# Optimization experiments

Measured on AMD Instinct MI355X. Metric: run time of the kernel, lower is better.

The kernel has to match this reference:

```python
import jax, jax.numpy as jnp
import numpy as np

WS = 7          # window_size
HEADS = 3
HD = 32         # head_dim
HIDDEN = 96
DISP = WS // 2  # 3
NEG_INF = float('-inf')


def _relative_indices():
    idx = np.array([[i, j] for i in range(WS) for j in range(WS)])
    rel = idx[None, :, :] - idx[:, None, :] + WS - 1  # [49,49,2], values in [0, 2*WS-2]
    return rel.astype(np.int32)


def _upper_lower_mask():
    m = np.zeros((WS * WS, WS * WS), dtype=np.float32)
    m[-DISP * WS:, :-DISP * WS] = NEG_INF
    m[:-DISP * WS, -DISP * WS:] = NEG_INF
    return m


def setup_inputs() -> dict:
    key = jax.random.key(0)
    ks = jax.random.split(key, 6)
    B, H, W = 32, 56, 56
    inner = HEADS * HD
    return {
        'x': jax.random.normal(ks[0], (B, H, W, HIDDEN), jnp.float32),
        'w_qkv': jax.random.normal(ks[1], (HIDDEN, inner * 3), jnp.float32) * 0.05,
        'b_qkv': jax.random.normal(ks[2], (inner * 3,), jnp.float32) * 0.05,
        'pos_embedding': jax.random.normal(ks[3], (2 * WS - 1, 2 * WS - 1), jnp.float32),
        'w_out': jax.random.normal(ks[4], (inner, HIDDEN), jnp.float32) * 0.05,
        'b_out': jax.random.normal(ks[5], (HIDDEN,), jnp.float32) * 0.05,
    }


def reference(x, w_qkv, b_qkv, pos_embedding, w_out, b_out):
    B, H, W, _ = x.shape
    nw_h, nw_w = H // WS, W // WS
    nw = nw_h * nw_w
    scale = HIDDEN ** (-0.5)  # original scales by hidden_dim**-0.5

    rel = jnp.asarray(_relative_indices())
    ul_mask = jnp.asarray(_upper_lower_mask())

    # cyclic shift
    xs = jnp.roll(x, (-DISP, -DISP), axis=(1, 2))
    qkv = xs @ w_qkv + b_qkv
    q, k, v = jnp.split(qkv, 3, axis=-1)

    def to_windows(e):
        # [B,H,W,heads*hd] -> [B,heads,nw,WS*WS,hd]
        e = e.reshape(B, nw_h, WS, nw_w, WS, HEADS, HD)
        e = e.transpose(0, 5, 1, 3, 2, 4, 6)
        return e.reshape(B, HEADS, nw, WS * WS, HD)

    q, k, v = to_windows(q), to_windows(k), to_windows(v)

    att = jnp.einsum('bhwid,bhwjd->bhwij', q, k) * scale
    att = att + pos_embedding[rel[:, :, 0], rel[:, :, 1]]
    # shifted: original only adds upper_lower_mask (right_left line is a no-op bug)
    att = att.at[:, :, -nw_w:].add(ul_mask)
    att = jax.nn.softmax(att, axis=-1)

    out = jnp.einsum('bhwij,bhwjd->bhwid', att, v)
    out = out.reshape(B, HEADS, nw_h, nw_w, WS, WS, HD)
    out = out.transpose(0, 2, 4, 3, 5, 1, 6).reshape(B, H, W, HEADS * HD)
    out = out @ w_out + b_out
    out = jnp.roll(out, (DISP, DISP), axis=(1, 2))
    return out
```

## Files before the change

kernel.cpp:

```cpp
#include <hip/hip_runtime.h>
#include <hip/hip_bf16.h>
#include <cmath>

using bf16 = __hip_bfloat16;
typedef __attribute__((ext_vector_type(8))) short short8;
typedef __attribute__((ext_vector_type(4))) float floatx4;

#define B_      32
#define HH      56
#define WW      56
#define HIDDEN  96
#define HEADS   3
#define HD      32
#define WS_     7
#define DISP    3
#define NWH     8
#define NWW     8
#define NW      64
#define WS2     49
#define NFRAG_QKV (3*6*3*64)
#define NFRAG_OUT (6*3*64)
#define NPEL      (2*64*64)

#if __has_builtin(__builtin_amdgcn_exp2f)
#define EXP2(x) __builtin_amdgcn_exp2f(x)
#else
#define EXP2(x) exp2f(x)
#endif

__device__ inline unsigned short bf16_bits(float f) {
  unsigned u = __float_as_uint(f);
  unsigned r = u + 0x7fffu + ((u >> 16) & 1u);
  return (unsigned short)(r >> 16);
}

__device__ inline unsigned cvtpk(float lo, float hi) {
  unsigned r;
  asm("v_cvt_pk_bf16_f32 %0, %1, %2" : "=v"(r) : "v"(lo), "v"(hi));
  return r;
}

__device__ inline unsigned short* swz(const unsigned short* plane, int row, int boff) {
  return (unsigned short*)((char*)plane + (row << 6) + (boff ^ ((row & 3) << 4)));
}

__global__ __launch_bounds__(256) void prep_kernel(
    const float* __restrict__ w_qkv, const float* __restrict__ w_out,
    const float* __restrict__ pos_emb,
    bf16* __restrict__ wfq, bf16* __restrict__ wfo, float* __restrict__ pelT) {
  int f = blockIdx.x * 256 + threadIdx.x;
  if (f < NFRAG_QKV) {
    int lane = f & 63, t = f >> 6;
    int kb = t % 3, t2 = t / 3, c6 = t2 % 6, ci = t2 / 6;
    int col = ci * 96 + c6 * 16 + (lane & 15);
    int k0 = kb * 32 + (lane >> 4) * 8;
    bf16 vals[8];
#pragma unroll
    for (int j = 0; j < 8; j++) vals[j] = __float2bfloat16(w_qkv[(k0 + j) * 288 + col]);
    *(short8*)&wfq[(size_t)f * 8] = *(const short8*)vals;
  } else if (f < NFRAG_QKV + NFRAG_OUT) {
    int fo = f - NFRAG_QKV;
    int lane = fo & 63, t = fo >> 6;
    int kb = t % 3, c6 = t / 3;
    int col = c6 * 16 + (lane & 15);
    int k0 = kb * 32 + (lane >> 4) * 8;
    bf16 vals[8];
#pragma unroll
    for (int j = 0; j < 8; j++) vals[j] = __float2bfloat16(w_out[(k0 + j) * 96 + col]);
    *(short8*)&wfo[(size_t)fo * 8] = *(const short8*)vals;
  } else {
    int p = f - (NFRAG_QKV + NFRAG_OUT);
    if (p < NPEL) {
      int mk = p >> 12, i = (p >> 6) & 63, j = p & 63;
      int iy = i / WS_, ix = i % WS_, jy = j / WS_, jx = j % WS_;
      int idx = (jy - iy + 6) * 13 + (jx - ix + 6);
      idx = idx < 0 ? 0 : (idx > 168 ? 168 : idx);
      bool live = (i < WS2) && (j < WS2) && !(mk && ((i >= 28) != (j >= 28)));
      pelT[p] = live ? pos_emb[idx] * 1.4426950408889634f : -1e30f;
    }
  }
}

__global__ __launch_bounds__(256, 4) void fused_swin_kernel(
    const float* __restrict__ x,
    const bf16* __restrict__ wfq, const bf16* __restrict__ wfo,
    const float* __restrict__ b_qkv, const float* __restrict__ b_out,
    const float* __restrict__ pelT, float* __restrict__ out) {

  __shared__ unsigned short slabA[3][64][32];
  __shared__ unsigned short slabB[3][64][32];
  __shared__ unsigned short vT[3][32][72];
  __shared__ unsigned tokoff[64];

  const int blk = blockIdx.x;
  const int nw = blk & 63, b = blk >> 6;
  const int wy = nw >> 3, wx = nw & 7;
  const int tid = threadIdx.x;
  const int lane = tid & 63, wv = tid >> 6;
  const int n_ = lane & 15, quad = lane >> 4;

  const short8* wfQ = (const short8*)wfq;
  short8 wcur0 = wfQ[(size_t)((wv * 3 + 0) * 64 + lane)];
  short8 wcur1 = wfQ[(size_t)((wv * 3 + 1) * 64 + lane)];
  short8 wcur2 = wfQ[(size_t)((wv * 3 + 2) * 64 + lane)];

  {
    const int rowp = tid >> 2, s0 = tid & 3;
    const bool haveRow = rowp < WS2;
    const float* xrow = x;
    if (haveRow) {
      const int py = rowp / WS_, px = rowp % WS_;
      int h = wy * WS_ + py + DISP; if (h >= HH) h -= HH;
      int w = wx * WS_ + px + DISP; if (w >= WW) w -= WW;
      const unsigned toff = (unsigned)(((b * HH + h) * WW + w) * HIDDEN);
      xrow = x + toff;
      if (s0 == 0) tokoff[rowp] = toff;
    }
#pragma unroll
    for (int p = 0; p < 6; p++) {
      const int seg = s0 + 4 * p;
      const int kb = seg >> 3;
      uint2 pk = (uint2){0u, 0u};
      if (haveRow) {
        const float4 xv = *(const float4*)&xrow[seg * 4];
        pk.x = cvtpk(xv.x, xv.y);
        pk.y = cvtpk(xv.z, xv.w);
      }
      *(uint2*)swz(&slabA[kb][0][0], rowp, (seg & 7) * 8) = pk;
    }
  }

  const bool maskedw = (nw >= NW - NWW);
  float pelv[4][4];
  {
    const float4* pt4 = (const float4*)&pelT[(maskedw ? 4096 : 0) + (16 * wv + n_) * 64];
#pragma unroll
    for (int jt = 0; jt < 4; jt++) {
      const float4 p4 = pt4[8 * (jt & 1) + (jt >> 1) + 2 * quad];
      pelv[jt][0] = p4.x; pelv[jt][1] = p4.y;
      pelv[jt][2] = p4.z; pelv[jt][3] = p4.w;
    }
  }
  __syncthreads();

  short8 af[4][3];
#pragma unroll
  for (int m = 0; m < 4; m++)
#pragma unroll
    for (int kb = 0; kb < 3; kb++)
      af[m][kb] = *(const short8*)swz(&slabA[kb][0][0], 16 * m + n_, quad * 16);
  __syncthreads();

  {
    const int rB = 32 * ((n_ >> 2) & 1) + 4 * (n_ >> 3) + (n_ & 3);
    int t = wv;
    while (t < 18) {
      const int tn = t + 4;
      short8 wn0 = wcur0, wn1 = wcur1, wn2 = wcur2;
      if (tn < 18) {
        wn0 = wfQ[(size_t)((tn * 3 + 0) * 64 + lane)];
        wn1 = wfQ[(size_t)((tn * 3 + 1) * 64 + lane)];
        wn2 = wfQ[(size_t)((tn * 3 + 2) * 64 + lane)];
      }
      const int ci = t / 6, c6 = t % 6, head = c6 >> 1;
      floatx4 acc[4];
      if (ci < 2) {
        const float4 bq = *(const float4*)&b_qkv[t * 16 + 4 * quad];
#pragma unroll
        for (int m = 0; m < 4; m++) acc[m] = (floatx4){bq.x, bq.y, bq.z, bq.w};
#pragma unroll
        for (int m = 0; m < 4; m++) {
          acc[m] = __builtin_amdgcn_mfma_f32_16x16x32_bf16(wcur0, af[m][0], acc[m], 0, 0, 0);
          acc[m] = __builtin_amdgcn_mfma_f32_16x16x32_bf16(wcur1, af[m][1], acc[m], 0, 0, 0);
          acc[m] = __builtin_amdgcn_mfma_f32_16x16x32_bf16(wcur2, af[m][2], acc[m], 0, 0, 0);
        }
        const int boff = ((c6 & 1) << 5) + quad * 8;
        if (ci == 0) {
#pragma unroll
          for (int m = 0; m < 4; m++) {
            uint2 st;
            st.x = cvtpk(acc[m][0], acc[m][1]);
            st.y = cvtpk(acc[m][2], acc[m][3]);
            *(uint2*)swz(&slabA[head][0][0], 16 * m + n_, boff) = st;
          }
        } else {
#pragma unroll
          for (int m = 0; m < 4; m++) {
            uint2 st;
            st.x = cvtpk(acc[m][0], acc[m][1]);
            st.y = cvtpk(acc[m][2], acc[m][3]);
            *(uint2*)swz(&slabB[head][0][0], rB + 8 * m, boff) = st;
          }
        }
      } else {
        const float bias = b_qkv[t * 16 + n_];
#pragma unroll
        for (int m = 0; m < 4; m++) acc[m] = (floatx4){bias, bias, bias, bias};
#pragma unroll
        for (int m = 0; m < 4; m++) {
          acc[m] = __builtin_amdgcn_mfma_f32_16x16x32_bf16(af[m][0], wcur0, acc[m], 0, 0, 0);
          acc[m] = __builtin_amdgcn_mfma_f32_16x16x32_bf16(af[m][1], wcur1, acc[m], 0, 0, 0);
          acc[m] = __builtin_amdgcn_mfma_f32_16x16x32_bf16(af[m][2], wcur2, acc[m], 0, 0, 0);
        }
        const int dc = ((c6 & 1) << 4) + n_;
#pragma unroll
        for (int m = 0; m < 4; m++) {
          uint2 st;
          st.x = cvtpk(acc[m][0], acc[m][1]);
          st.y = cvtpk(acc[m][2], acc[m][3]);
          *(uint2*)&vT[head][dc][16 * m + 4 * quad] = st;
        }
      }
      wcur0 = wn0; wcur1 = wn1; wcur2 = wn2;
      t = tn;
    }
  }
  __syncthreads();

  const float scale2 = 0.147244446f;
  const floatx4 zero4 = (floatx4){0.f, 0.f, 0.f, 0.f};

  short8 aq[3];
#pragma unroll
  for (int h = 0; h < HEADS; h++)
    aq[h] = *(const short8*)swz(&slabA[h][0][0], 16 * wv + n_, quad * 16);
  floatx4 sAcc[3][4];
  __builtin_amdgcn_s_setprio(1);
#pragma unroll
  for (int h = 0; h < HEADS; h++)
#pragma unroll
    for (int jt = 0; jt < 4; jt++) {
      const short8 bk = *(const short8*)swz(&slabB[h][0][0], 16 * jt + n_, quad * 16);
      sAcc[h][jt] = __builtin_amdgcn_mfma_f32_16x16x32_bf16(bk, aq[h], zero4, 0, 0, 0);
    }
  __builtin_amdgcn_s_setprio(0);

  uint2 ost[3][2];
#pragma unroll
  for (int h = 0; h < HEADS; h++) {
    float ei[4][4];
    float s = 0.f;
#pragma unroll
    for (int jt = 0; jt < 4; jt++)
#pragma unroll
      for (int r = 0; r < 4; r++) {
        const float e = EXP2(fmaf(sAcc[h][jt][r], scale2, pelv[jt][r]));
        ei[jt][r] = e;
        s += e;
      }
    s += __shfl_xor(s, 16);
    s += __shfl_xor(s, 32);
    const float invq = s > 0.f ? __builtin_amdgcn_rcpf(s) : 0.f;

    unsigned pk2[4][2];
#pragma unroll
    for (int jt = 0; jt < 4; jt++) {
      pk2[jt][0] = cvtpk(ei[jt][0], ei[jt][1]);
      pk2[jt][1] = cvtpk(ei[jt][2], ei[jt][3]);
    }
    short8 apf[2];
#pragma unroll
    for (int kc = 0; kc < 2; kc++) {
      union { unsigned u[4]; short8 s8; } fu;
      fu.u[0] = pk2[kc][0];
      fu.u[1] = pk2[kc][1];
      fu.u[2] = pk2[2 + kc][0];
      fu.u[3] = pk2[2 + kc][1];
      apf[kc] = fu.s8;
    }

    floatx4 oAcc[2] = {zero4, zero4};
    __builtin_amdgcn_s_setprio(1);
#pragma unroll
    for (int nt = 0; nt < 2; nt++)
#pragma unroll
      for (int kc = 0; kc < 2; kc++) {
        const short8 bv = *(const short8*)&vT[h][16 * nt + n_][32 * kc + quad * 8];
        oAcc[nt] = __builtin_amdgcn_mfma_f32_16x16x32_bf16(bv, apf[kc], oAcc[nt], 0, 0, 0);
      }
    __builtin_amdgcn_s_setprio(0);
#pragma unroll
    for (int nt = 0; nt < 2; nt++) {
      ost[h][nt].x = cvtpk(oAcc[nt][0] * invq, oAcc[nt][1] * invq);
      ost[h][nt].y = cvtpk(oAcc[nt][2] * invq, oAcc[nt][3] * invq);
    }
  }

#pragma unroll
  for (int h = 0; h < HEADS; h++)
#pragma unroll
    for (int nt = 0; nt < 2; nt++)
      *(uint2*)swz(&slabA[h][0][0], 16 * wv + n_, nt * 32 + quad * 8) = ost[h][nt];
  __syncthreads();

  short8 af2[4][3];
#pragma unroll
  for (int m = 0; m < 4; m++)
#pragma unroll
    for (int kb = 0; kb < 3; kb++)
      af2[m][kb] = *(const short8*)swz(&slabA[kb][0][0], 16 * m + n_, quad * 16);

  unsigned obase[4][4];
#pragma unroll
  for (int m = 0; m < 4; m++)
#pragma unroll
    for (int r = 0; r < 4; r++)
      obase[m][r] = tokoff[16 * m + 4 * quad + r] + (unsigned)n_;

  const short8* wfO = (const short8*)wfo;
  {
    int t = wv;
    short8 oc0 = wfO[(size_t)((t * 3 + 0) * 64 + lane)];
    short8 oc1 = wfO[(size_t)((t * 3 + 1) * 64 + lane)];
    short8 oc2 = wfO[(size_t)((t * 3 + 2) * 64 + lane)];
    while (t < 6) {
      const int tn = t + 4;
      short8 on0 = oc0, on1 = oc1, on2 = oc2;
      if (tn < 6) {
        on0 = wfO[(size_t)((tn * 3 + 0) * 64 + lane)];
        on1 = wfO[(size_t)((tn * 3 + 1) * 64 + lane)];
        on2 = wfO[(size_t)((tn * 3 + 2) * 64 + lane)];
      }
      const float bias = b_out[t * 16 + n_];
      floatx4 acc[4];
#pragma unroll
      for (int m = 0; m < 4; m++) acc[m] = (floatx4){bias, bias, bias, bias};
#pragma unroll
      for (int m = 0; m < 4; m++) {
        acc[m] = __builtin_amdgcn_mfma_f32_16x16x32_bf16(af2[m][0], oc0, acc[m], 0, 0, 0);
        acc[m] = __builtin_amdgcn_mfma_f32_16x16x32_bf16(af2[m][1], oc1, acc[m], 0, 0, 0);
        acc[m] = __builtin_amdgcn_mfma_f32_16x16x32_bf16(af2[m][2], oc2, acc[m], 0, 0, 0);
      }
#pragma unroll
      for (int m = 0; m < 4; m++)
#pragma unroll
        for (int r = 0; r < 4; r++) {
          if (16 * m + 4 * quad + r < WS2)
            out[(size_t)obase[m][r] + t * 16] = acc[m][r];
        }
      oc0 = on0; oc1 = on1; oc2 = on2;
      t = tn;
    }
  }
}

extern "C" void kernel_launch(void* const* d_in, const int* in_sizes, int n_in,
                              void* d_out, int out_size, void* d_ws, size_t ws_size,
                              hipStream_t stream) {
  const float* x     = (const float*)d_in[0];
  const float* w_qkv = (const float*)d_in[1];
  const float* b_qkv = (const float*)d_in[2];
  const float* pos   = (const float*)d_in[3];
  const float* w_out = (const float*)d_in[4];
  const float* b_out = (const float*)d_in[5];
  float* out = (float*)d_out;

  bf16* wfq = (bf16*)d_ws;
  bf16* wfo = wfq + (size_t)NFRAG_QKV * 8;
  float* pelT = (float*)((char*)d_ws + (size_t)(NFRAG_QKV + NFRAG_OUT) * 8 * 2);

  prep_kernel<<<50, 256, 0, stream>>>(w_qkv, w_out, pos, wfq, wfo, pelT);
  fused_swin_kernel<<<B_ * NW, 256, 0, stream>>>(x, wfq, wfo, b_qkv, b_out, pelT, out);
}
```

Measured before the change: 119.2 us.

## Split output projection by token rows per wave and drop block barrier

```diff
diff --git a/kernel.cpp b/kernel.cpp
--- a/kernel.cpp
+++ b/kernel.cpp
@@ -291,55 +291,40 @@
 #pragma unroll
     for (int nt = 0; nt < 2; nt++)
       *(uint2*)swz(&slabA[h][0][0], 16 * wv + n_, nt * 32 + quad * 8) = ost[h][nt];
-  __syncthreads();
-
-  short8 af2[4][3];
-#pragma unroll
-  for (int m = 0; m < 4; m++)
-#pragma unroll
-    for (int kb = 0; kb < 3; kb++)
-      af2[m][kb] = *(const short8*)swz(&slabA[kb][0][0], 16 * m + n_, quad * 16);
-
-  unsigned obase[4][4];
-#pragma unroll
-  for (int m = 0; m < 4; m++)
-#pragma unroll
-    for (int r = 0; r < 4; r++)
-      obase[m][r] = tokoff[16 * m + 4 * quad + r] + (unsigned)n_;
+
+  short8 af2[3];
+#pragma unroll
+  for (int kb = 0; kb < 3; kb++)
+    af2[kb] = *(const short8*)swz(&slabA[kb][0][0], 16 * wv + n_, quad * 16);
+
+  const int baserow = 16 * wv + 4 * quad;
+  unsigned obase[4];
+#pragma unroll
+  for (int r = 0; r < 4; r++)
+    obase[r] = tokoff[baserow + r] + (unsigned)n_;
 
   const short8* wfO = (const short8*)wfo;
   {
-    int t = wv;
-    short8 oc0 = wfO[(size_t)((t * 3 + 0) * 64 + lane)];
-    short8 oc1 = wfO[(size_t)((t * 3 + 1) * 64 + lane)];
-    short8 oc2 = wfO[(size_t)((t * 3 + 2) * 64 + lane)];
-    while (t < 6) {
-      const int tn = t + 4;
+    short8 oc0 = wfO[(size_t)((0 * 3 + 0) * 64 + lane)];
+    short8 oc1 = wfO[(size_t)((0 * 3 + 1) * 64 + lane)];
+    short8 oc2 = wfO[(size_t)((0 * 3 + 2) * 64 + lane)];
+    for (int t = 0; t < 6; t++) {
       short8 on0 = oc0, on1 = oc1, on2 = oc2;
-      if (tn < 6) {
-        on0 = wfO[(size_t)((tn * 3 + 0) * 64 + lane)];
-        on1 = wfO[(size_t)((tn * 3 + 1) * 64 + lane)];
-        on2 = wfO[(size_t)((tn * 3 + 2) * 64 + lane)];
+      if (t < 5) {
+        on0 = wfO[(size_t)(((t + 1) * 3 + 0) * 64 + lane)];
+        on1 = wfO[(size_t)(((t + 1) * 3 + 1) * 64 + lane)];
+        on2 = wfO[(size_t)(((t + 1) * 3 + 2) * 64 + lane)];
       }
       const float bias = b_out[t * 16 + n_];
-      floatx4 acc[4];
-#pragma unroll
-      for (int m = 0; m < 4; m++) acc[m] = (floatx4){bias, bias, bias, bias};
-#pragma unroll
-      for (int m = 0; m < 4; m++) {
-        acc[m] = __builtin_amdgcn_mfma_f32_16x16x32_bf16(af2[m][0], oc0, acc[m], 0, 0, 0);
-        acc[m] = __builtin_amdgcn_mfma_f32_16x16x32_bf16(af2[m][1], oc1, acc[m], 0, 0, 0);
-        acc[m] = __builtin_amdgcn_mfma_f32_16x16x32_bf16(af2[m][2], oc2, acc[m], 0, 0, 0);
-      }
-#pragma unroll
-      for (int m = 0; m < 4; m++)
-#pragma unroll
-        for (int r = 0; r < 4; r++) {
-          if (16 * m + 4 * quad + r < WS2)
-            out[(size_t)obase[m][r] + t * 16] = acc[m][r];
-        }
+      floatx4 acc = (floatx4){bias, bias, bias, bias};
+      acc = __builtin_amdgcn_mfma_f32_16x16x32_bf16(af2[0], oc0, acc, 0, 0, 0);
+      acc = __builtin_amdgcn_mfma_f32_16x16x32_bf16(af2[1], oc1, acc, 0, 0, 0);
+      acc = __builtin_amdgcn_mfma_f32_16x16x32_bf16(af2[2], oc2, acc, 0, 0, 0);
+#pragma unroll
+      for (int r = 0; r < 4; r++)
+        if (baserow + r < WS2)
+          out[(size_t)obase[r] + t * 16] = acc[r];
       oc0 = on0; oc1 = on1; oc2 = on2;
-      t = tn;
     }
   }
 }
```

After: 115.5 us (median of 2 runs). 3.1% less time.
